# Kernel optimization log

Measured on AMD Instinct MI355X. Metric: run time of the kernel, lower is better.

## Reference

```python
import jax, jax.numpy as jnp
import numpy as np

BOUND = 1.2


def _ste_sign(v, bound):
    # forward: sign(v); backward: d clamp(v,-bound,bound)/dv (straight-through estimator)
    clipped = jnp.clip(v, -bound, bound)
    return jax.lax.stop_gradient(jnp.sign(v) - clipped) + clipped


def setup_inputs() -> dict:
    key = jax.random.key(0)
    kx, kw = jax.random.split(key)
    x = jax.random.normal(kx, (32, 128, 112, 112), dtype=jnp.float32)
    # xavier_normal_ with gain=2.0: std = gain * sqrt(2/(fan_in+fan_out)), fan = C*k*k
    fan = 128 * 3 * 3
    std = 2.0 * np.sqrt(2.0 / (fan + fan))
    weights = jax.random.normal(kw, (128, 128, 3, 3), dtype=jnp.float32) * std
    return {"x": x, "weights": weights}


def reference(x, weights):
    # Binarize activations and weights with STE (training-mode math of BConv)
    xb = _ste_sign(x, BOUND)
    wb = _ste_sign(weights, BOUND)
    # conv2d, NCHW input, OIHW weights, stride 1, padding 1, dilation 1
    out = jax.lax.conv_general_dilated(
        xb, wb,
        window_strides=(1, 1),
        padding=((1, 1), (1, 1)),
        lhs_dilation=(1, 1),
        rhs_dilation=(1, 1),
        dimension_numbers=("NCHW", "OIHW", "NCHW"),
        feature_group_count=1,
    )
    return out
```

## Files before the change

kernel.cpp:

```cpp
#include <hip/hip_runtime.h>
#include <cstdint>
#include <cstddef>

#define NIMG 32
#define C    128
#define OC   128
#define HW   112
#define HWSZ (HW * HW)
#define NTAP 9
#define PHW  114
#define XROW (PHW * C)
#define XIMG (PHW * XROW)
#define XQ_BYTES ((size_t)NIMG * XIMG)
#define AWQ_BYTES ((size_t)8 * 9 * 2 * 64 * 16)

typedef int v4i __attribute__((ext_vector_type(4)));

__device__ __forceinline__ uint32_t sign_byte(uint32_t bits) {
    return ((bits >> 31) * 0xFEu) ^ 1u;
}

__global__ void fill_border(uint8_t* __restrict__ xq) {
    int tid = blockIdx.x * blockDim.x + threadIdx.x;
    int n = tid / 3616, u = tid % 3616;
    size_t off;
    if (u < 912)        off = (size_t)u * 16;
    else if (u < 1824)  off = (size_t)113 * XROW + (size_t)(u - 912) * 16;
    else {
        int j = u - 1824;
        int r = (j >> 4) + 1;
        int side = (j >> 3) & 1;
        int cu = j & 7;
        off = (size_t)r * XROW + (size_t)side * (113 * C) + (size_t)cu * 16;
    }
    *(uint4*)(xq + (size_t)n * XIMG + off) = make_uint4(0u, 0u, 0u, 0u);
}

__global__ __launch_bounds__(256) void pack_x_cl(const float* __restrict__ x,
                                                 uint8_t* __restrict__ xq) {
    __shared__ __align__(16) uint8_t slds[2 * 112 * 144];
    int n = blockIdx.x / 56, hp = blockIdx.x % 56;
    int h0 = hp * 2;

    int task = threadIdx.x;
    if (task < 224) {
        int r = task / 112, rem = task % 112;
        int word = rem / 28, pxg = rem % 28;
        const float* xp = x + ((size_t)(n * C + word * 32)) * HWSZ
                            + (size_t)(h0 + r) * HW + pxg * 4;
        uint32_t dw[4][8];
        #pragma unroll
        for (int i = 0; i < 8; ++i) {
            uint32_t a0 = 0, a1 = 0, a2 = 0, a3 = 0;
            #pragma unroll
            for (int b = 0; b < 4; ++b) {
                float4 v = *reinterpret_cast<const float4*>(xp + (size_t)(i * 4 + b) * HWSZ);
                a0 |= sign_byte(__float_as_uint(v.x)) << (8 * b);
                a1 |= sign_byte(__float_as_uint(v.y)) << (8 * b);
                a2 |= sign_byte(__float_as_uint(v.z)) << (8 * b);
                a3 |= sign_byte(__float_as_uint(v.w)) << (8 * b);
            }
            dw[0][i] = a0; dw[1][i] = a1; dw[2][i] = a2; dw[3][i] = a3;
        }
        #pragma unroll
        for (int j = 0; j < 4; ++j) {
            uint8_t* sp = &slds[(size_t)((r * 112) + pxg * 4 + j) * 144 + word * 32];
            *(uint4*)sp        = make_uint4(dw[j][0], dw[j][1], dw[j][2], dw[j][3]);
            *(uint4*)(sp + 16) = make_uint4(dw[j][4], dw[j][5], dw[j][6], dw[j][7]);
        }
    }
    __syncthreads();

    uint8_t* dst = xq + (size_t)n * XIMG + (size_t)(h0 + 1) * XROW + C;
    #pragma unroll
    for (int rep = 0; rep < 7; ++rep) {
        int u = threadIdx.x + rep * 256;
        int row = u / 896, i = u % 896;
        *(uint4*)(dst + (size_t)row * XROW + (size_t)i * 16) =
            *(const uint4*)&slds[(size_t)(row * 112 + (i >> 3)) * 144 + (i & 7) * 16];
    }
}

__global__ void pack_w_frag(const float* __restrict__ w, uint32_t* __restrict__ awq) {
    int tid = blockIdx.x * blockDim.x + threadIdx.x;
    int d = tid & 3, l = (tid >> 2) & 63, f = tid >> 8;
    int ks = f & 1, tf = f >> 1;
    int tap = tf % 9, o16 = tf / 9;
    int o = o16 * 16 + (l & 15);
    int cb = ks * 64 + ((l >> 4) & 3) * 16 + d * 4;
    uint32_t acc = 0;
    #pragma unroll
    for (int jj = 0; jj < 4; ++jj) {
        uint32_t bits = __float_as_uint(w[(size_t)(o * C + cb + jj) * NTAP + tap]);
        acc |= sign_byte(bits) << (8 * jj);
    }
    awq[tid] = acc;
}

__global__ __launch_bounds__(256, 2) void bconv_mfma(const uint8_t* __restrict__ xq,
                                                     const uint8_t* __restrict__ awq,
                                                     float* __restrict__ out) {
    __shared__ __align__(16) uint8_t sxq[3 * XROW];
    int bid = blockIdx.x;
    int swz = (bid & 7) * 448 + (bid >> 3);
    int n = swz / HW, h = swz % HW;

    const uint8_t* src = xq + (size_t)n * XIMG + (size_t)h * XROW;
    #pragma unroll
    for (int rep = 0; rep < 11; ++rep) {
        int u = threadIdx.x + rep * 256;
        if (u < 2736) {
            int pix = (u >> 3) % PHW;
            uint4 v = *(const uint4*)(src + (size_t)u * 16);
            int a = (u * 16) ^ ((pix & 7) << 4);
            *(uint4*)&sxq[a] = v;
        }
    }

    int wv = threadIdx.x >> 6, l = threadIdx.x & 63;
    int l15 = l & 15, lk = (l >> 4) * 16;

    v4i A[2][9][2];
    #pragma unroll
    for (int ot = 0; ot < 2; ++ot)
        #pragma unroll
        for (int tap = 0; tap < 9; ++tap)
            #pragma unroll
            for (int ks = 0; ks < 2; ++ks) {
                int f = ((wv * 2 + ot) * 9 + tap) * 2 + ks;
                A[ot][tap][ks] = *(const v4i*)(awq + (size_t)f * 1024 + (size_t)l * 16);
            }
    __syncthreads();

    float* outb = out + ((size_t)n * OC + wv * 32) * HWSZ + h * HW;

    for (int nt = 0; nt < 7; ++nt) {
        int w0 = nt * 16;
        int ad[3][2];
        #pragma unroll
        for (int kw = 0; kw < 3; ++kw) {
            int pix = w0 + l15 + kw;
            int x4 = (pix & 7) << 4;
            int base = pix * C;
            ad[kw][0] = base + (lk ^ x4);
            ad[kw][1] = base + ((lk + 64) ^ x4);
        }
        v4i acc0 = {0, 0, 0, 0}, acc1 = {0, 0, 0, 0};
        #pragma unroll
        for (int kh = 0; kh < 3; ++kh)
            #pragma unroll
            for (int kw = 0; kw < 3; ++kw)
                #pragma unroll
                for (int ks = 0; ks < 2; ++ks) {
                    v4i b = *(const v4i*)&sxq[kh * XROW + ad[kw][ks]];
                    acc0 = __builtin_amdgcn_mfma_i32_16x16x64_i8(
                               A[0][kh * 3 + kw][ks], b, acc0, 0, 0, 0);
                    acc1 = __builtin_amdgcn_mfma_i32_16x16x64_i8(
                               A[1][kh * 3 + kw][ks], b, acc1, 0, 0, 0);
                }
        #pragma unroll
        for (int r = 0; r < 4; ++r) {
            int oof = ((l >> 4) << 2) + r;
            outb[(size_t)oof * HWSZ + w0 + l15]        = (float)acc0[r];
            outb[(size_t)(oof + 16) * HWSZ + w0 + l15] = (float)acc1[r];
        }
    }
}

extern "C" void kernel_launch(void* const* d_in, const int* in_sizes, int n_in,
                              void* d_out, int out_size, void* d_ws, size_t ws_size,
                              hipStream_t stream) {
    const float* x   = (const float*)d_in[0];
    const float* wts = (const float*)d_in[1];
    float* out = (float*)d_out;
    uint8_t* ws = (uint8_t*)d_ws;

    uint8_t*  xq  = ws;
    uint32_t* awq = (uint32_t*)(ws + XQ_BYTES);

    hipLaunchKernelGGL(fill_border, dim3(NIMG * 3616 / 256), dim3(256), 0, stream, xq);
    hipLaunchKernelGGL(pack_w_frag, dim3(144), dim3(256), 0, stream, wts, awq);
    hipLaunchKernelGGL(pack_x_cl, dim3(NIMG * 56), dim3(256), 0, stream, x, xq);
    hipLaunchKernelGGL(bconv_mfma, dim3(NIMG * HW), dim3(256), 0, stream,
                       xq, (const uint8_t*)awq, out);
}
```

Before: 140.1 us.

## Switch binary conv to 32x32x32 int8 MFMA over two output rows per block

Replaces the pair of 16x16x64 int8 MFMAs per step with a single 32x32x32 MFMA per wave covering 32 output channels by 32 pixels. Each block now handles two output rows, staging four padded input rows in LDS and halving the grid. The weight fragment packing is re-laid out to match the new A-operand layout. The aim is to cut input-row reloads per output row and reduce LDS B-operand traffic per MAC, at the cost of more LDS per block and a different output-store pattern.

New measurement: 141.9 us. Within noise of the previous version (+1.2%).

```diff
diff --git a/kernel.cpp b/kernel.cpp
--- a/kernel.cpp
+++ b/kernel.cpp
@@ -12,9 +12,10 @@
 #define XROW (PHW * C)
 #define XIMG (PHW * XROW)
 #define XQ_BYTES ((size_t)NIMG * XIMG)
-#define AWQ_BYTES ((size_t)8 * 9 * 2 * 64 * 16)
+#define AWQ_BYTES ((size_t)4 * 9 * 4 * 64 * 16)
 
-typedef int v4i __attribute__((ext_vector_type(4)));
+typedef int v4i  __attribute__((ext_vector_type(4)));
+typedef int v16i __attribute__((ext_vector_type(16)));
 
 __device__ __forceinline__ uint32_t sign_byte(uint32_t bits) {
     return ((bits >> 31) * 0xFEu) ^ 1u;
@@ -84,10 +85,10 @@
 __global__ void pack_w_frag(const float* __restrict__ w, uint32_t* __restrict__ awq) {
     int tid = blockIdx.x * blockDim.x + threadIdx.x;
     int d = tid & 3, l = (tid >> 2) & 63, f = tid >> 8;
-    int ks = f & 1, tf = f >> 1;
-    int tap = tf % 9, o16 = tf / 9;
-    int o = o16 * 16 + (l & 15);
-    int cb = ks * 64 + ((l >> 4) & 3) * 16 + d * 4;
+    int ks = f & 3, tf = f >> 2;
+    int tap = tf % 9, wv = tf / 9;
+    int o = wv * 32 + (l & 31);
+    int cb = ks * 32 + ((l >> 5) & 1) * 16 + d * 4;
     uint32_t acc = 0;
     #pragma unroll
     for (int jj = 0; jj < 4; ++jj) {
@@ -100,16 +101,17 @@
 __global__ __launch_bounds__(256, 2) void bconv_mfma(const uint8_t* __restrict__ xq,
                                                      const uint8_t* __restrict__ awq,
                                                      float* __restrict__ out) {
-    __shared__ __align__(16) uint8_t sxq[3 * XROW];
+    __shared__ __align__(16) uint8_t sxq[4 * XROW];
     int bid = blockIdx.x;
-    int swz = (bid & 7) * 448 + (bid >> 3);
-    int n = swz / HW, h = swz % HW;
+    int swz = (bid & 7) * 224 + (bid >> 3);
+    int n = swz / 56, hp = swz % 56;
+    int h0 = hp * 2;
 
-    const uint8_t* src = xq + (size_t)n * XIMG + (size_t)h * XROW;
+    const uint8_t* src = xq + (size_t)n * XIMG + (size_t)h0 * XROW;
     #pragma unroll
-    for (int rep = 0; rep < 11; ++rep) {
+    for (int rep = 0; rep < 15; ++rep) {
         int u = threadIdx.x + rep * 256;
-        if (u < 2736) {
+        if (u < 3648) {
             int pix = (u >> 3) % PHW;
             uint4 v = *(const uint4*)(src + (size_t)u * 16);
             int a = (u * 16) ^ ((pix & 7) << 4);
@@ -118,51 +120,52 @@
     }
 
     int wv = threadIdx.x >> 6, l = threadIdx.x & 63;
-    int l15 = l & 15, lk = (l >> 4) * 16;
+    int l31 = l & 31, lk = (l >> 5) * 16;
 
-    v4i A[2][9][2];
+    v4i A[9][4];
     #pragma unroll
-    for (int ot = 0; ot < 2; ++ot)
+    for (int tap = 0; tap < 9; ++tap)
         #pragma unroll
-        for (int tap = 0; tap < 9; ++tap)
-            #pragma unroll
-            for (int ks = 0; ks < 2; ++ks) {
-                int f = ((wv * 2 + ot) * 9 + tap) * 2 + ks;
-                A[ot][tap][ks] = *(const v4i*)(awq + (size_t)f * 1024 + (size_t)l * 16);
-            }
+        for (int ks = 0; ks < 4; ++ks) {
+            int f = (wv * 9 + tap) * 4 + ks;
+            A[tap][ks] = *(const v4i*)(awq + (size_t)f * 1024 + (size_t)l * 16);
+        }
     __syncthreads();
 
-    float* outb = out + ((size_t)n * OC + wv * 32) * HWSZ + h * HW;
+    float* outb = out + ((size_t)n * OC + wv * 32) * HWSZ + (size_t)h0 * HW;
 
     for (int nt = 0; nt < 7; ++nt) {
-        int w0 = nt * 16;
-        int ad[3][2];
+        int p = nt * 32 + l31;
+        int rl = (p >= HW) ? 1 : 0;
+        int w = p - rl * HW;
+
+        int ad[3][4];
         #pragma unroll
         for (int kw = 0; kw < 3; ++kw) {
-            int pix = w0 + l15 + kw;
-            int x4 = (pix & 7) << 4;
-            int base = pix * C;
-            ad[kw][0] = base + (lk ^ x4);
-            ad[kw][1] = base + ((lk + 64) ^ x4);
+            int col = w + kw;
+            int x4 = (col & 7) << 4;
+            int b0 = rl * XROW + col * C;
+            #pragma unroll
+            for (int ks = 0; ks < 4; ++ks)
+                ad[kw][ks] = b0 + ((ks * 32 + lk) ^ x4);
         }
-        v4i acc0 = {0, 0, 0, 0}, acc1 = {0, 0, 0, 0};
+
+        v16i acc = {0,0,0,0,0,0,0,0,0,0,0,0,0,0,0,0};
         #pragma unroll
         for (int kh = 0; kh < 3; ++kh)
             #pragma unroll
             for (int kw = 0; kw < 3; ++kw)
                 #pragma unroll
-                for (int ks = 0; ks < 2; ++ks) {
+                for (int ks = 0; ks < 4; ++ks) {
                     v4i b = *(const v4i*)&sxq[kh * XROW + ad[kw][ks]];
-                    acc0 = __builtin_amdgcn_mfma_i32_16x16x64_i8(
-                               A[0][kh * 3 + kw][ks], b, acc0, 0, 0, 0);
-                    acc1 = __builtin_amdgcn_mfma_i32_16x16x64_i8(
-                               A[1][kh * 3 + kw][ks], b, acc1, 0, 0, 0);
+                    acc = __builtin_amdgcn_mfma_i32_32x32x32_i8(
+                              A[kh * 3 + kw][ks], b, acc, 0, 0, 0);
                 }
+
         #pragma unroll
-        for (int r = 0; r < 4; ++r) {
-            int oof = ((l >> 4) << 2) + r;
-            outb[(size_t)oof * HWSZ + w0 + l15]        = (float)acc0[r];
-            outb[(size_t)(oof + 16) * HWSZ + w0 + l15] = (float)acc1[r];
+        for (int r = 0; r < 16; ++r) {
+            int oof = (r & 3) + 8 * (r >> 2) + 4 * (l >> 5);
+            outb[(size_t)oof * HWSZ + rl * HW + w] = (float)acc[r];
         }
     }
 }
@@ -181,6 +184,6 @@
     hipLaunchKernelGGL(fill_border, dim3(NIMG * 3616 / 256), dim3(256), 0, stream, xq);
     hipLaunchKernelGGL(pack_w_frag, dim3(144), dim3(256), 0, stream, wts, awq);
     hipLaunchKernelGGL(pack_x_cl, dim3(NIMG * 56), dim3(256), 0, stream, x, xq);
-    hipLaunchKernelGGL(bconv_mfma, dim3(NIMG * HW), dim3(256), 0, stream,
+    hipLaunchKernelGGL(bconv_mfma, dim3(NIMG * 56), dim3(256), 0, stream,
                        xq, (const uint8_t*)awq, out);
 }
```
